# Kernel tuning notes

Hardware: AMD Instinct MI355X
Metric: run time of the kernel (lower is better)

Reference implementation:

```python
import jax, jax.numpy as jnp
import numpy as np

B, H_C, W_C = 4, 256, 256        # coarse mask logits
C, H_F, W_F = 128, 512, 512      # fine feature map
N_POINTS = 8192
HIDDEN = 256


def _grid_sample_bilinear(img, grid):
    """Bilinear grid_sample, align_corners=False, zeros padding.
    img: [C,H,W]; grid: [N,2] with (x,y) in [-1,1]. Returns [N,C]."""
    Ci, H, W = img.shape
    x = ((grid[:, 0] + 1.0) * W - 1.0) * 0.5
    y = ((grid[:, 1] + 1.0) * H - 1.0) * 0.5
    x0 = jnp.floor(x); y0 = jnp.floor(y)
    x1 = x0 + 1.0; y1 = y0 + 1.0
    wx1 = x - x0; wx0 = 1.0 - wx1
    wy1 = y - y0; wy0 = 1.0 - wy1

    def gather(xi, yi):
        valid = (xi >= 0) & (xi < W) & (yi >= 0) & (yi < H)
        xc = jnp.clip(xi, 0, W - 1).astype(jnp.int32)
        yc = jnp.clip(yi, 0, H - 1).astype(jnp.int32)
        v = img[:, yc, xc]                       # [C,N]
        return v * valid.astype(img.dtype)

    out = (gather(x0, y0) * (wx0 * wy0)
           + gather(x1, y0) * (wx1 * wy0)
           + gather(x0, y1) * (wx0 * wy1)
           + gather(x1, y1) * (wx1 * wy1))       # [C,N]
    return out.T                                  # [N,C]


def setup_inputs() -> dict:
    key = jax.random.key(0)
    k1, k2, k3, k4 = jax.random.split(key, 4)
    coarse_logits = jax.random.normal(k1, (B, 1, H_C, W_C), dtype=jnp.float32)
    fine_feat = jax.random.normal(k2, (B, C, H_F, W_F), dtype=jnp.float32)
    W1 = jax.random.normal(k3, (C + 1, HIDDEN), dtype=jnp.float32) * (1.0 / np.sqrt(C + 1))
    b1 = jnp.zeros((HIDDEN,), dtype=jnp.float32)
    W2 = jax.random.normal(k4, (HIDDEN, 1), dtype=jnp.float32) * (1.0 / np.sqrt(HIDDEN))
    b2 = jnp.zeros((1,), dtype=jnp.float32)
    return {"coarse_logits": coarse_logits, "fine_feat": fine_feat,
            "W1": W1, "b1": b1, "W2": W2, "b2": b2, "num_points": N_POINTS}


def reference(coarse_logits, fine_feat, W1, b1, W2, b2, num_points):
    b, _, h, w = coarse_logits.shape
    # uncertainty = -|logits|  (calculate_uncertainty)
    unc = -jnp.abs(coarse_logits[:, 0])                       # [B,h,w]
    _, idx = jax.lax.top_k(unc.reshape(b, -1), num_points)    # [B,N]
    # pixel-center normalized coords (sampling_points eval branch): (x,y) in [0,1]
    h_step, w_step = 1.0 / h, 1.0 / w
    px = w_step / 2.0 + (idx % w).astype(jnp.float32) * w_step
    py = h_step / 2.0 + (idx // w).astype(jnp.float32) * h_step
    grid = 2.0 * jnp.stack([px, py], axis=-1) - 1.0           # [B,N,2] in [-1,1]
    # point_sample: bilinear gather of fine features at sampled points
    fine_pts = jax.vmap(_grid_sample_bilinear)(fine_feat, grid)   # [B,N,C]
    # point_sample_by_idx: gather coarse logits at flat indices
    coarse_flat = coarse_logits.reshape(b, -1)                 # [B,h*w]
    coarse_pts = jnp.take_along_axis(coarse_flat, idx, axis=1)[..., None]  # [B,N,1]
    # point head MLP on concat(fine, coarse)
    feats = jnp.concatenate([fine_pts, coarse_pts], axis=-1)   # [B,N,C+1]
    hid = jax.nn.relu(jnp.einsum('bnf,fk->bnk', feats, W1) + b1)
    refined = jnp.einsum('bnk,ko->bno', hid, W2) + b2          # [B,N,1]
    # scatter refined logits back into the coarse map at sampled indices
    out_flat = coarse_flat.at[jnp.arange(b)[:, None], idx].set(refined[..., 0])
    return out_flat.reshape(b, 1, h, w)
```

## Files before the change

kernel.cpp:

```cpp
#include <hip/hip_runtime.h>
#include <stdint.h>

#define B_ 4
#define HC 256
#define WC 256
#define C_ 128
#define HF 512
#define WF 512
#define NPTS 8192
#define HIDDEN_ 256
#define NPIX (HC*WC)
#define PPB 32
#define FSTRIDE 132

__global__ void pr_copy_kernel(const float4* __restrict__ src, float4* __restrict__ dst, int n4) {
    int i = blockIdx.x * blockDim.x + threadIdx.x;
    if (i < n4) dst[i] = src[i];
}

__global__ __launch_bounds__(1024) void pr_select_kernel(const float* __restrict__ coarse,
                                                         int* __restrict__ sel) {
    int b = blockIdx.x;
    const float* cb = coarse + (size_t)b * NPIX;
    int tid = threadIdx.x;
    __shared__ unsigned hist[256];
    __shared__ unsigned s_prefix;
    __shared__ int s_remk;
    __shared__ unsigned warp_eq[16];
    __shared__ unsigned s_eqbase;
    __shared__ unsigned s_outcnt;

    if (tid == 0) { s_prefix = 0u; s_remk = NPTS; s_eqbase = 0u; s_outcnt = 0u; }

    for (int pass = 0; pass < 4; ++pass) {
        if (tid < 256) hist[tid] = 0u;
        __syncthreads();
        unsigned prefix = s_prefix;
        int shift = 24 - 8 * pass;
        for (int i = tid; i < NPIX; i += 1024) {
            unsigned k = __float_as_uint(cb[i]) & 0x7fffffffu;
            bool cond = (pass == 0) || ((k >> (shift + 8)) == prefix);
            if (cond) atomicAdd(&hist[(k >> shift) & 0xffu], 1u);
        }
        __syncthreads();
        if (tid == 0) {
            unsigned c = 0; int remk = s_remk; int chosen = 0;
            for (int bin = 0; bin < 256; ++bin) {
                unsigned h = hist[bin];
                if ((unsigned)remk <= c + h) { chosen = bin; break; }
                c += h;
            }
            s_prefix = (s_prefix << 8) | (unsigned)chosen;
            s_remk = remk - (int)c;
        }
        __syncthreads();
    }

    unsigned T = s_prefix;
    unsigned need_eq = (unsigned)s_remk;
    int lane = tid & 63, wid = tid >> 6;
    for (int base = 0; base < NPIX; base += 1024) {
        int i = base + tid;
        unsigned k = __float_as_uint(cb[i]) & 0x7fffffffu;
        bool lt = (k < T);
        bool eq = (k == T);
        unsigned long long m = __ballot(eq);
        if (lane == 0) warp_eq[wid] = (unsigned)__popcll(m);
        __syncthreads();
        unsigned wbase = 0, tot = 0;
        for (int w = 0; w < 16; ++w) { unsigned h = warp_eq[w]; if (w < wid) wbase += h; tot += h; }
        unsigned rank = s_eqbase + wbase + (unsigned)__popcll(m & ((1ull << lane) - 1ull));
        bool take = lt || (eq && rank < need_eq);
        if (take) {
            unsigned pos = atomicAdd(&s_outcnt, 1u);
            sel[b * NPTS + pos] = i;
        }
        __syncthreads();
        if (tid == 0) s_eqbase += tot;
    }
}

__global__ __launch_bounds__(256) void pr_mlp_kernel(
    const float* __restrict__ coarse, const float* __restrict__ fine,
    const float* __restrict__ W1, const float* __restrict__ b1,
    const float* __restrict__ W2, const float* __restrict__ b2,
    const int* __restrict__ sel, float* __restrict__ out) {

    __shared__ float feats[PPB * FSTRIDE];
    __shared__ int sidx[PPB];
    __shared__ float red[PPB][4];

    int tid = threadIdx.x;
    const int bpb = NPTS / PPB;
    int b = blockIdx.x / bpb;
    int pbase = (blockIdx.x % bpb) * PPB;

    if (tid < PPB) sidx[tid] = sel[b * NPTS + pbase + tid];
    __syncthreads();

    const float* fb = fine + (size_t)b * C_ * HF * WF;
    int c = tid & 127;
    int ph = tid >> 7;
    for (int it = 0; it < PPB / 2; ++it) {
        int p = 2 * it + ph;
        int id = sidx[p];
        int ix = id & (WC - 1), iy = id >> 8;
        const float* a = fb + (size_t)c * (HF * WF) + (size_t)(2 * iy) * WF + 2 * ix;
        float2 r0 = *(const float2*)a;
        float2 r1 = *(const float2*)(a + WF);
        feats[p * FSTRIDE + c] = 0.25f * ((r0.x + r0.y) + (r1.x + r1.y));
    }
    if (tid < PPB) feats[tid * FSTRIDE + 128] = coarse[(size_t)b * NPIX + sidx[tid]];
    __syncthreads();

    int j = tid;
    float acc[PPB];
    float b1j = b1[j];
#pragma unroll
    for (int p = 0; p < PPB; ++p) acc[p] = b1j;

    const float4* fs4 = (const float4*)feats;
    for (int f4 = 0; f4 < 32; ++f4) {
        float w0 = W1[(4 * f4 + 0) * HIDDEN_ + j];
        float w1 = W1[(4 * f4 + 1) * HIDDEN_ + j];
        float w2 = W1[(4 * f4 + 2) * HIDDEN_ + j];
        float w3 = W1[(4 * f4 + 3) * HIDDEN_ + j];
#pragma unroll
        for (int p = 0; p < PPB; ++p) {
            float4 fv = fs4[p * (FSTRIDE / 4) + f4];
            acc[p] = fmaf(fv.x, w0, acc[p]);
            acc[p] = fmaf(fv.y, w1, acc[p]);
            acc[p] = fmaf(fv.z, w2, acc[p]);
            acc[p] = fmaf(fv.w, w3, acc[p]);
        }
    }
    {
        float w128 = W1[128 * HIDDEN_ + j];
#pragma unroll
        for (int p = 0; p < PPB; ++p) acc[p] = fmaf(feats[p * FSTRIDE + 128], w128, acc[p]);
    }

    float w2j = W2[j];
    int lane = tid & 63, wid = tid >> 6;
#pragma unroll
    for (int p = 0; p < PPB; ++p) {
        float v = fmaxf(acc[p], 0.0f) * w2j;
        v += __shfl_down(v, 32, 64);
        v += __shfl_down(v, 16, 64);
        v += __shfl_down(v, 8, 64);
        v += __shfl_down(v, 4, 64);
        v += __shfl_down(v, 2, 64);
        v += __shfl_down(v, 1, 64);
        if (lane == 0) red[p][wid] = v;
    }
    __syncthreads();
    if (tid < PPB) {
        float r = red[tid][0] + red[tid][1] + red[tid][2] + red[tid][3] + b2[0];
        out[(size_t)b * NPIX + sidx[tid]] = r;
    }
}

extern "C" void kernel_launch(void* const* d_in, const int* in_sizes, int n_in,
                              void* d_out, int out_size, void* d_ws, size_t ws_size,
                              hipStream_t stream) {
    const float* coarse = (const float*)d_in[0];
    const float* fine   = (const float*)d_in[1];
    const float* W1     = (const float*)d_in[2];
    const float* b1     = (const float*)d_in[3];
    const float* W2     = (const float*)d_in[4];
    const float* b2     = (const float*)d_in[5];
    float* out = (float*)d_out;
    int* sel = (int*)d_ws;

    int n4 = B_ * NPIX / 4;
    pr_copy_kernel<<<(n4 + 255) / 256, 256, 0, stream>>>((const float4*)coarse, (float4*)out, n4);
    pr_select_kernel<<<B_, 1024, 0, stream>>>(coarse, sel);
    pr_mlp_kernel<<<B_ * (NPTS / PPB), 256, 0, stream>>>(coarse, fine, W1, b1, W2, b2, sel, out);
}
```

Baseline: 850.9 us.

## Vectorize radix select, warp-aggregate histograms, batch gathers, halve points per block

The top-k select kernel now reads float4 chunks, aggregates first-pass histogram atomics per warp via ballot matching, replaces the serial single-thread bin scan with a parallel prefix scan, and emits selected indices with a deterministic ballot-based compaction instead of shared atomics. The MLP kernel halves points per block to launch more blocks, issues all fine-feature loads before any reductions so more memory requests are in flight, and partially unrolls the W1 loop. These changes target the serial, latency-bound select kernel and the gather latency in the MLP kernel. The cost is more block launches, with W1 loaded once per block and so reloaded twice as often, plus more register pressure.

```diff
diff --git a/kernel.cpp b/kernel.cpp
--- a/kernel.cpp
+++ b/kernel.cpp
@@ -10,7 +10,7 @@
 #define NPTS 8192
 #define HIDDEN_ 256
 #define NPIX (HC*WC)
-#define PPB 32
+#define PPB 16
 #define FSTRIDE 132
 
 __global__ void pr_copy_kernel(const float4* __restrict__ src, float4* __restrict__ dst, int n4) {
@@ -23,60 +23,151 @@
     int b = blockIdx.x;
     const float* cb = coarse + (size_t)b * NPIX;
     int tid = threadIdx.x;
+    int lane = tid & 63, wid = tid >> 6;
+
     __shared__ unsigned hist[256];
     __shared__ unsigned s_prefix;
     __shared__ int s_remk;
-    __shared__ unsigned warp_eq[16];
-    __shared__ unsigned s_eqbase;
-    __shared__ unsigned s_outcnt;
-
-    if (tid == 0) { s_prefix = 0u; s_remk = NPTS; s_eqbase = 0u; s_outcnt = 0u; }
+    __shared__ unsigned wsum[16];
+    __shared__ unsigned s_chosen, s_cless;
+    __shared__ unsigned warp_eq[16], warp_take[16];
+    __shared__ unsigned s_eqbase, s_outbase;
+
+    if (tid == 0) { s_prefix = 0u; s_remk = NPTS; }
 
     for (int pass = 0; pass < 4; ++pass) {
         if (tid < 256) hist[tid] = 0u;
         __syncthreads();
         unsigned prefix = s_prefix;
+        int remk = s_remk;
         int shift = 24 - 8 * pass;
-        for (int i = tid; i < NPIX; i += 1024) {
-            unsigned k = __float_as_uint(cb[i]) & 0x7fffffffu;
-            bool cond = (pass == 0) || ((k >> (shift + 8)) == prefix);
-            if (cond) atomicAdd(&hist[(k >> shift) & 0xffu], 1u);
-        }
-        __syncthreads();
-        if (tid == 0) {
-            unsigned c = 0; int remk = s_remk; int chosen = 0;
-            for (int bin = 0; bin < 256; ++bin) {
-                unsigned h = hist[bin];
-                if ((unsigned)remk <= c + h) { chosen = bin; break; }
-                c += h;
+
+        if (pass == 0) {
+            for (int i = 4 * tid; i < NPIX; i += 4096) {
+                float4 v = *(const float4*)(cb + i);
+                unsigned bins[4];
+                bins[0] = (__float_as_uint(v.x) & 0x7fffffffu) >> 24;
+                bins[1] = (__float_as_uint(v.y) & 0x7fffffffu) >> 24;
+                bins[2] = (__float_as_uint(v.z) & 0x7fffffffu) >> 24;
+                bins[3] = (__float_as_uint(v.w) & 0x7fffffffu) >> 24;
+#pragma unroll
+                for (int e = 0; e < 4; ++e) {
+                    unsigned bin = bins[e];
+                    unsigned long long am = ~0ull;
+                    while (am) {
+                        int leader = __ffsll((unsigned long long)am) - 1;
+                        unsigned lbin = __shfl(bin, leader, 64);
+                        unsigned long long match = __ballot(bin == lbin);
+                        if (lane == leader) atomicAdd(&hist[lbin], (unsigned)__popcll(match));
+                        am &= ~match;
+                    }
+                }
             }
-            s_prefix = (s_prefix << 8) | (unsigned)chosen;
-            s_remk = remk - (int)c;
-        }
+        } else {
+            for (int i = 4 * tid; i < NPIX; i += 4096) {
+                float4 v = *(const float4*)(cb + i);
+                unsigned k0 = __float_as_uint(v.x) & 0x7fffffffu;
+                unsigned k1 = __float_as_uint(v.y) & 0x7fffffffu;
+                unsigned k2 = __float_as_uint(v.z) & 0x7fffffffu;
+                unsigned k3 = __float_as_uint(v.w) & 0x7fffffffu;
+                if ((k0 >> (shift + 8)) == prefix) atomicAdd(&hist[(k0 >> shift) & 0xffu], 1u);
+                if ((k1 >> (shift + 8)) == prefix) atomicAdd(&hist[(k1 >> shift) & 0xffu], 1u);
+                if ((k2 >> (shift + 8)) == prefix) atomicAdd(&hist[(k2 >> shift) & 0xffu], 1u);
+                if ((k3 >> (shift + 8)) == prefix) atomicAdd(&hist[(k3 >> shift) & 0xffu], 1u);
+            }
+        }
+        __syncthreads();
+
+        unsigned h = 0, incl = 0;
+        if (tid < 256) {
+            h = hist[tid];
+            incl = h;
+#pragma unroll
+            for (int d = 1; d < 64; d <<= 1) {
+                unsigned y = __shfl_up(incl, d, 64);
+                if (lane >= d) incl += y;
+            }
+            if (lane == 63) wsum[wid] = incl;
+        }
+        __syncthreads();
+        if (tid < 256) {
+            unsigned base = 0;
+            for (int w = 0; w < wid; ++w) base += wsum[w];
+            unsigned inc = base + incl;
+            unsigned exc = inc - h;
+            if ((unsigned)remk > exc && (unsigned)remk <= inc) { s_chosen = (unsigned)tid; s_cless = exc; }
+        }
+        __syncthreads();
+        if (tid == 0) { s_prefix = (s_prefix << 8) | s_chosen; s_remk = remk - (int)s_cless; }
         __syncthreads();
     }
 
     unsigned T = s_prefix;
     unsigned need_eq = (unsigned)s_remk;
-    int lane = tid & 63, wid = tid >> 6;
-    for (int base = 0; base < NPIX; base += 1024) {
-        int i = base + tid;
-        unsigned k = __float_as_uint(cb[i]) & 0x7fffffffu;
-        bool lt = (k < T);
-        bool eq = (k == T);
-        unsigned long long m = __ballot(eq);
-        if (lane == 0) warp_eq[wid] = (unsigned)__popcll(m);
-        __syncthreads();
-        unsigned wbase = 0, tot = 0;
-        for (int w = 0; w < 16; ++w) { unsigned h = warp_eq[w]; if (w < wid) wbase += h; tot += h; }
-        unsigned rank = s_eqbase + wbase + (unsigned)__popcll(m & ((1ull << lane) - 1ull));
-        bool take = lt || (eq && rank < need_eq);
-        if (take) {
-            unsigned pos = atomicAdd(&s_outcnt, 1u);
-            sel[b * NPTS + pos] = i;
-        }
-        __syncthreads();
-        if (tid == 0) s_eqbase += tot;
+    if (tid == 0) { s_eqbase = 0u; s_outbase = 0u; }
+    __syncthreads();
+
+    unsigned long long ltmask = (1ull << lane) - 1ull;
+    for (int base = 0; base < NPIX; base += 4096) {
+        int i0 = base + 4 * tid;
+        float4 v = *(const float4*)(cb + i0);
+        unsigned k[4];
+        k[0] = __float_as_uint(v.x) & 0x7fffffffu;
+        k[1] = __float_as_uint(v.y) & 0x7fffffffu;
+        k[2] = __float_as_uint(v.z) & 0x7fffffffu;
+        k[3] = __float_as_uint(v.w) & 0x7fffffffu;
+        bool lt[4], eq[4];
+        unsigned long long me[4];
+        unsigned weq = 0;
+#pragma unroll
+        for (int e = 0; e < 4; ++e) {
+            lt[e] = k[e] < T;
+            eq[e] = k[e] == T;
+            me[e] = __ballot(eq[e]);
+            weq += (unsigned)__popcll(me[e]);
+        }
+        if (lane == 0) warp_eq[wid] = weq;
+        __syncthreads();
+
+        unsigned eqwb = 0, eqtot = 0;
+        for (int w = 0; w < 16; ++w) { unsigned hh = warp_eq[w]; if (w < wid) eqwb += hh; eqtot += hh; }
+        unsigned lt_lanes_eq = 0;
+#pragma unroll
+        for (int e = 0; e < 4; ++e) lt_lanes_eq += (unsigned)__popcll(me[e] & ltmask);
+        unsigned ebase = s_eqbase + eqwb + lt_lanes_eq;
+
+        bool take[4];
+        unsigned long long mt[4];
+        unsigned self_eq = 0;
+#pragma unroll
+        for (int e = 0; e < 4; ++e) {
+            unsigned eqrank = ebase + self_eq;
+            take[e] = lt[e] || (eq[e] && eqrank < need_eq);
+            self_eq += eq[e] ? 1u : 0u;
+        }
+        unsigned wtk = 0;
+#pragma unroll
+        for (int e = 0; e < 4; ++e) {
+            mt[e] = __ballot(take[e]);
+            wtk += (unsigned)__popcll(mt[e]);
+        }
+        if (lane == 0) warp_take[wid] = wtk;
+        __syncthreads();
+
+        unsigned twb = 0, ttot = 0;
+        for (int w = 0; w < 16; ++w) { unsigned hh = warp_take[w]; if (w < wid) twb += hh; ttot += hh; }
+        unsigned lt_lanes_tk = 0;
+#pragma unroll
+        for (int e = 0; e < 4; ++e) lt_lanes_tk += (unsigned)__popcll(mt[e] & ltmask);
+        unsigned tbase = s_outbase + twb + lt_lanes_tk;
+        unsigned self_tk = 0;
+#pragma unroll
+        for (int e = 0; e < 4; ++e) {
+            if (take[e]) sel[b * NPTS + (int)(tbase + self_tk)] = i0 + e;
+            self_tk += take[e] ? 1u : 0u;
+        }
+        __syncthreads();
+        if (tid == 0) { s_eqbase += eqtot; s_outbase += ttot; }
     }
 }
 
@@ -86,7 +177,7 @@
     const float* __restrict__ W2, const float* __restrict__ b2,
     const int* __restrict__ sel, float* __restrict__ out) {
 
-    __shared__ float feats[PPB * FSTRIDE];
+    __shared__ __align__(16) float feats[PPB * FSTRIDE];
     __shared__ int sidx[PPB];
     __shared__ float red[PPB][4];
 
@@ -98,17 +189,24 @@
     if (tid < PPB) sidx[tid] = sel[b * NPTS + pbase + tid];
     __syncthreads();
 
-    const float* fb = fine + (size_t)b * C_ * HF * WF;
+    const float* fb = fine + (size_t)b * (C_ * HF * WF);
     int c = tid & 127;
     int ph = tid >> 7;
-    for (int it = 0; it < PPB / 2; ++it) {
-        int p = 2 * it + ph;
+
+    float2 r0[PPB / 2], r1[PPB / 2];
+#pragma unroll
+    for (int k = 0; k < PPB / 2; ++k) {
+        int p = 2 * k + ph;
         int id = sidx[p];
         int ix = id & (WC - 1), iy = id >> 8;
         const float* a = fb + (size_t)c * (HF * WF) + (size_t)(2 * iy) * WF + 2 * ix;
-        float2 r0 = *(const float2*)a;
-        float2 r1 = *(const float2*)(a + WF);
-        feats[p * FSTRIDE + c] = 0.25f * ((r0.x + r0.y) + (r1.x + r1.y));
+        r0[k] = *(const float2*)a;
+        r1[k] = *(const float2*)(a + WF);
+    }
+#pragma unroll
+    for (int k = 0; k < PPB / 2; ++k) {
+        int p = 2 * k + ph;
+        feats[p * FSTRIDE + c] = 0.25f * ((r0[k].x + r0[k].y) + (r1[k].x + r1[k].y));
     }
     if (tid < PPB) feats[tid * FSTRIDE + 128] = coarse[(size_t)b * NPIX + sidx[tid]];
     __syncthreads();
@@ -120,6 +218,7 @@
     for (int p = 0; p < PPB; ++p) acc[p] = b1j;
 
     const float4* fs4 = (const float4*)feats;
+#pragma unroll 4
     for (int f4 = 0; f4 < 32; ++f4) {
         float w0 = W1[(4 * f4 + 0) * HIDDEN_ + j];
         float w1 = W1[(4 * f4 + 1) * HIDDEN_ + j];
```

Result: faster. 797.0 us (-6.3%).
